# Optimization experiments

Measured on AMD Instinct MI355X. Metric: run time of the kernel, lower is better.

Reference implementation:

```python
import jax, jax.numpy as jnp
import numpy as np

H = 512  # hidden size (layer_size in the torch module)


def setup_inputs() -> dict:
    key = jax.random.key(0)
    ks = jax.random.split(key, 12)
    B, T = 512, 128
    s = 1.0 / np.sqrt(H)  # torch default LSTM/Linear init range
    def u(k, shape):
        return jax.random.uniform(k, shape, jnp.float32, -s, s)
    return {
        "x": jax.random.normal(ks[0], (B, T, 1), jnp.float32),
        "x_time": jax.random.normal(ks[1], (B, T), jnp.float32),
        "y_time": jax.random.normal(ks[2], (B, T), jnp.float32),
        # layer 0: input_size=1
        "w_ih0": u(ks[3], (4 * H, 1)),
        "w_hh0": u(ks[4], (4 * H, H)),
        "b_ih0": u(ks[5], (4 * H,)),
        "b_hh0": u(ks[6], (4 * H,)),
        # layer 1: input_size=H
        "w_ih1": u(ks[7], (4 * H, H)),
        "w_hh1": u(ks[8], (4 * H, H)),
        "b_ih1": u(ks[9], (4 * H,)),
        "b_hh1": u(ks[10], (4 * H,)),
        # output head Linear(512, 1)
        "w_lin": u(ks[11], (1, H)),
        "b_lin": jnp.zeros((1,), jnp.float32),
    }


def _cell(x, h, c, w_ih, w_hh, b):
    # torch LSTM gate order: i, f, g, o
    g = x @ w_ih.T + h @ w_hh.T + b
    i, f, gg, o = jnp.split(g, 4, axis=-1)
    c = jax.nn.sigmoid(f) * c + jax.nn.sigmoid(i) * jnp.tanh(gg)
    h = jax.nn.sigmoid(o) * jnp.tanh(c)
    return h, c


def reference(x, x_time, y_time, w_ih0, w_hh0, b_ih0, b_hh0,
              w_ih1, w_hh1, b_ih1, b_hh1, w_lin, b_lin):
    # x: [B, T, 1]; x_time / y_time are unused (as in the torch module)
    B, T, _ = x.shape
    b0 = b_ih0 + b_hh0
    b1 = b_ih1 + b_hh1

    def step(state, x_t):  # x_t: [B, 1]
        h1, c1, h2, c2 = state
        h1, c1 = _cell(x_t, h1, c1, w_ih0, w_hh0, b0)
        h2, c2 = _cell(h1, h2, c2, w_ih1, w_hh1, b1)
        return (h1, c1, h2, c2), h2

    z = jnp.zeros((B, H), x.dtype)
    state = (z, z, z, z)
    # phase 1: run the 2-layer LSTM over the full input sequence (first loop iter)
    state, _ = jax.lax.scan(step, state, jnp.swapaxes(x, 0, 1))
    y0 = state[3] @ w_lin.T + b_lin  # [B, 1] first prediction

    def ar_step(carry, _):
        st, y = carry
        st, h2 = step(st, y)
        y_new = h2 @ w_lin.T + b_lin
        return (st, y_new), y_new

    _, ys = jax.lax.scan(ar_step, (state, y0), None, length=T - 1)  # [T-1, B, 1]
    preds = jnp.concatenate([y0[None], ys], axis=0)  # [T, B, 1]
    return jnp.transpose(preds, (1, 0, 2))  # [B, T, 1]
```

## Files before the change

kernel.cpp:

```cpp
#include <hip/hip_runtime.h>
#include <math.h>
#include <stdint.h>


namespace {
constexpr int NH  = 512;
constexpr int NT  = 128;
constexpr int NB  = 512;
}

typedef __attribute__((ext_vector_type(8))) short bf16x8;
typedef __attribute__((ext_vector_type(4))) float f32x4;
typedef __attribute__((ext_vector_type(4))) unsigned int u32x4;

__global__ void ReLSTM_18940805775611_kernel() {}

__device__ __forceinline__ unsigned short lstm9_f2b(float f) {
    union { float f; uint32_t i; } v; v.f = f;
    const uint32_t r = v.i + 0x7FFFu + ((v.i >> 16) & 1u);
    return (unsigned short)(r >> 16);
}
__device__ __forceinline__ float lstm9_sig(float x) {
    return 1.0f / (1.0f + expf(-x));
}

__global__ void lstm9_mark(float* out) {
    const int i = blockIdx.x * blockDim.x + threadIdx.x;
    if (i < NB * NT) out[i] = 2.03125f;
}

__global__ void lstm9_prep(
    const float* whh0, const float* wih1, const float* whh1,
    const float* bih0, const float* bhh0, const float* bih1, const float* bhh1,
    unsigned short* wb0, unsigned short* wb1i, unsigned short* wb1h,
    float* bsum0, float* bsum1,
    unsigned short* hz, int* flags)
{
    const size_t stride = (size_t)gridDim.x * blockDim.x;
    const size_t i0 = (size_t)blockIdx.x * blockDim.x + threadIdx.x;
    const size_t NW = (size_t)4 * NH * NH;
    for (size_t i = i0; i < NW; i += stride) {
        wb0 [i] = lstm9_f2b(whh0[i]);
        wb1i[i] = lstm9_f2b(wih1[i]);
        wb1h[i] = lstm9_f2b(whh1[i]);
    }
    for (size_t i = i0; i < (size_t)4 * NH; i += stride) {
        bsum0[i] = bih0[i] + bhh0[i];
        bsum1[i] = bih1[i] + bhh1[i];
    }
    for (size_t i = i0; i < (size_t)4 * NB * NH; i += stride) hz[i] = 0;
    for (size_t i = i0; i < (size_t)2 * 256 * 8 * 32; i += stride) flags[i] = 0;
}

__device__ __forceinline__ void lstm9_ldA(u32x4& d, const unsigned short* p) {
    asm volatile("global_load_dwordx4 %0, %1, off sc0 sc1"
                 : "=v"(d) : "v"(p) : "memory");
}
__device__ __forceinline__ void lstm9_ldP(u32x4& d, const float* p) {
    asm volatile("global_load_dwordx4 %0, %1, off sc0 sc1"
                 : "=v"(d) : "v"(p) : "memory");
}
#define LSTM9_W8(N, a,b,c,d,e,f,g,h) \
    asm volatile("s_waitcnt vmcnt(" #N ")" \
        : "+v"(a),"+v"(b),"+v"(c),"+v"(d),"+v"(e),"+v"(f),"+v"(g),"+v"(h) :: "memory")
#define LSTM9_WAIT2(a,b) \
    asm volatile("s_waitcnt vmcnt(0)" : "+v"(a),"+v"(b) :: "memory")
__device__ __forceinline__ void lstm9_stH(unsigned short* p, unsigned short v) {
    unsigned int x = v;
    asm volatile("global_store_short %0, %1, off sc0 sc1" :: "v"(p), "v"(x) : "memory");
}
__device__ __forceinline__ void lstm9_stF(float* p, float v) {
    asm volatile("global_store_dword %0, %1, off sc0 sc1" :: "v"(p), "v"(v) : "memory");
}
__device__ __forceinline__ void lstm9_stI(int* p, int v) {
    asm volatile("global_store_dword %0, %1, off sc0 sc1" :: "v"(p), "v"(v) : "memory");
}
__device__ __forceinline__ void lstm9_drain() {
    asm volatile("s_waitcnt vmcnt(0)" ::: "memory");
}

__device__ __forceinline__ void lstm9_waitgrp(const int* base) {
    if (threadIdx.x < 64) {
        const int sl = (int)threadIdx.x & 31;
        for (;;) {
            int f;
            asm volatile("global_load_dword %0, %1, off sc0 sc1\n\t"
                         "s_waitcnt vmcnt(0)"
                         : "=v"(f) : "v"(base + sl) : "memory");
            if (__all(f != 0)) break;
            __builtin_amdgcn_s_sleep(2);
        }
    }
    __syncthreads();
}
__device__ __forceinline__ void lstm9_waitgrp2(const int* baseA, const int* baseB) {
    if (threadIdx.x < 64) {
        const int sl = (int)threadIdx.x & 31;
        const int* p = ((threadIdx.x < 32) ? baseA : baseB) + sl;
        for (;;) {
            int f;
            asm volatile("global_load_dword %0, %1, off sc0 sc1\n\t"
                         "s_waitcnt vmcnt(0)"
                         : "=v"(f) : "v"(p) : "memory");
            if (__all(f != 0)) break;
            __builtin_amdgcn_s_sleep(2);
        }
    }
    __syncthreads();
}

#define BFR0(gt, kk) (*(const bf16x8*)&Bsh0[gt][kk][lane][0])
#define BFR1(gt, kk) (*(const bf16x8*)&Bsh1[gt][kk][lane][0])
#define WHR(gt, kk)  (*(const bf16x8*)&whr[(gt) * 16 + (kk)])

__global__ __launch_bounds__(256, 1) void lstm9_persist(
    const float* __restrict__ xin, float* __restrict__ outf,
    const unsigned short* __restrict__ wb0,
    const unsigned short* __restrict__ wb1i,
    const unsigned short* __restrict__ wb1h,
    const float* __restrict__ bsum0, const float* __restrict__ bsum1,
    const float* __restrict__ wih0f, const float* __restrict__ wlinf,
    const float* __restrict__ blinf,
    unsigned short* h1a, unsigned short* h1b,
    unsigned short* h2a, unsigned short* h2b,
    float* parts, int* flags)
{
    __shared__ unsigned short Bsh0[4][16][64][8];
    __shared__ unsigned short Bsh1[4][16][64][8];
    __shared__ float redsh[64][17];
    __shared__ float ysh[64];

    const int tid  = threadIdx.x;
    const int lane = tid & 63;
    const int wv   = tid >> 6;
    const int quad = lane >> 4;
    const int ln15 = lane & 15;
    const int bid  = blockIdx.x;
    const int jt = (bid & 7) * 4 + ((bid >> 3) & 3);
    const int g  = bid >> 5;
    const int j0 = jt * 16;
    const int m0 = g * 64;
    const int rowA = m0 + wv * 16 + ln15;
    const int mb   = m0 + wv * 16 + quad * 4;
    const int jv   = j0 + ln15;

    for (int idx = tid; idx < 4 * 16 * 64; idx += 256) {
        const int gt = idx >> 10;
        const int ks = (idx >> 6) & 15;
        const int l  = idx & 63;
        const int row = l & 15, q = l >> 4;
        const size_t go = ((size_t)(gt * NH + j0 + row)) * NH + ks * 32 + q * 8;
        *(u32x4*)&Bsh0[gt][ks][l][0] = *(const u32x4*)(wb0  + go);
        *(u32x4*)&Bsh1[gt][ks][l][0] = *(const u32x4*)(wb1i + go);
    }
    u32x4 whr[64];
    #pragma unroll
    for (int gt = 0; gt < 4; ++gt) {
        #pragma unroll
        for (int ks = 0; ks < 16; ++ks)
            whr[gt * 16 + ks] = *(const u32x4*)(
                wb1h + ((size_t)(gt * NH + j0 + ln15)) * NH + ks * 32 + quad * 8);
    }
    __syncthreads();

    const float b0i = bsum0[jv],          b0f = bsum0[NH + jv];
    const float b0g = bsum0[2 * NH + jv], b0o = bsum0[3 * NH + jv];
    const float wxi = wih0f[jv],          wxf = wih0f[NH + jv];
    const float wxg = wih0f[2 * NH + jv], wxo = wih0f[3 * NH + jv];
    const float b1i = bsum1[jv],          b1f = bsum1[NH + jv];
    const float b1g = bsum1[2 * NH + jv], b1o = bsum1[3 * NH + jv];
    const float wl_ = wlinf[jv];
    const float bl_ = blinf[0];

    float c1r[4] = {0.f, 0.f, 0.f, 0.f};
    float c2r[4] = {0.f, 0.f, 0.f, 0.f};

    unsigned short* h1p[2] = { h1a, h1b };
    unsigned short* h2p[2] = { h2a, h2b };
    int* flagA = flags;
    int* flagB = flags + 256 * 8 * 32;

    u32x4 rP[8], rQ[8];

    for (int t = 0; t < 256; ++t) {
        const unsigned short* h1rd = h1p[t & 1];
        unsigned short*       h1wr = h1p[(t + 1) & 1];
        const unsigned short* h2rd = h2p[t & 1];
        unsigned short*       h2wr = h2p[(t + 1) & 1];

        if (t != 255) {
            #pragma unroll
            for (int ks = 0; ks < 8; ++ks)
                lstm9_ldA(rP[ks], h1rd + (size_t)rowA * NH + ks * 32 + quad * 8);
            #pragma unroll
            for (int ks = 0; ks < 8; ++ks)
                lstm9_ldA(rQ[ks], h1rd + (size_t)rowA * NH + (8 + ks) * 32 + quad * 8);
        }

        float xv[4] = {0.f, 0.f, 0.f, 0.f};
        if (t < 128) {
            #pragma unroll
            for (int r = 0; r < 4; ++r)
                xv[r] = xin[(size_t)(mb + r) * NT + t];
        } else {
            lstm9_waitgrp(flagB + ((t - 1) * 8 + g) * 32);
            const float* pslot = parts + (size_t)((t - 1) & 1) * NB * 32;
            {
                const int row = tid >> 2, q = tid & 3;
                u32x4 v0, v1;
                lstm9_ldP(v0, pslot + (size_t)(m0 + row) * 32 + q * 8);
                lstm9_ldP(v1, pslot + (size_t)(m0 + row) * 32 + q * 8 + 4);
                LSTM9_WAIT2(v0, v1);
                const float* f0 = (const float*)&v0;
                const float* f1 = (const float*)&v1;
                redsh[row][q] = f0[0] + f0[1] + f0[2] + f0[3]
                              + f1[0] + f1[1] + f1[2] + f1[3];
            }
            __syncthreads();
            if (tid < 64) {
                const float y = bl_ + redsh[tid][0] + redsh[tid][1]
                                    + redsh[tid][2] + redsh[tid][3];
                ysh[tid] = y;
                if (jt == 0)
                    outf[(size_t)(m0 + tid) * NT + (t - 128)] = y;
            }
            __syncthreads();
            if (t == 255) break;
            #pragma unroll
            for (int r = 0; r < 4; ++r)
                xv[r] = ysh[wv * 16 + quad * 4 + r];
        }

        f32x4 a0 = {0.f, 0.f, 0.f, 0.f};
        f32x4 a1 = a0, a2 = a0, a3 = a0;
        LSTM9_W8(8, rP[0], rP[1], rP[2], rP[3], rP[4], rP[5], rP[6], rP[7]);
        #pragma unroll
        for (int ks = 0; ks < 8; ++ks) {
            const bf16x8 af = *(const bf16x8*)&rP[ks];
            a0 = __builtin_amdgcn_mfma_f32_16x16x32_bf16(af, BFR0(0, ks), a0, 0, 0, 0);
            a1 = __builtin_amdgcn_mfma_f32_16x16x32_bf16(af, BFR0(1, ks), a1, 0, 0, 0);
            a2 = __builtin_amdgcn_mfma_f32_16x16x32_bf16(af, BFR0(2, ks), a2, 0, 0, 0);
            a3 = __builtin_amdgcn_mfma_f32_16x16x32_bf16(af, BFR0(3, ks), a3, 0, 0, 0);
        }
        LSTM9_W8(0, rQ[0], rQ[1], rQ[2], rQ[3], rQ[4], rQ[5], rQ[6], rQ[7]);
        #pragma unroll
        for (int ks = 0; ks < 8; ++ks) {
            const bf16x8 af = *(const bf16x8*)&rQ[ks];
            a0 = __builtin_amdgcn_mfma_f32_16x16x32_bf16(af, BFR0(0, 8 + ks), a0, 0, 0, 0);
            a1 = __builtin_amdgcn_mfma_f32_16x16x32_bf16(af, BFR0(1, 8 + ks), a1, 0, 0, 0);
            a2 = __builtin_amdgcn_mfma_f32_16x16x32_bf16(af, BFR0(2, 8 + ks), a2, 0, 0, 0);
            a3 = __builtin_amdgcn_mfma_f32_16x16x32_bf16(af, BFR0(3, 8 + ks), a3, 0, 0, 0);
        }

        #pragma unroll
        for (int r = 0; r < 4; ++r) {
            const float gi = a0[r] + fmaf(xv[r], wxi, b0i);
            const float gf = a1[r] + fmaf(xv[r], wxf, b0f);
            const float gg = a2[r] + fmaf(xv[r], wxg, b0g);
            const float go = a3[r] + fmaf(xv[r], wxo, b0o);
            float cv = c1r[r];
            cv = lstm9_sig(gf) * cv + lstm9_sig(gi) * tanhf(gg);
            c1r[r] = cv;
            lstm9_stH(h1wr + (size_t)(mb + r) * NH + jv,
                      lstm9_f2b(lstm9_sig(go) * tanhf(cv)));
        }
        lstm9_drain();
        __syncthreads();
        if (tid == 0) lstm9_stI(flagA + (t * 8 + g) * 32 + jt, 1);

        if (t < 128) {
            const int* bA = flagA + (t * 8 + g) * 32;
            const int* bB = (t >= 1) ? (flagB + ((t - 1) * 8 + g) * 32) : bA;
            lstm9_waitgrp2(bA, bB);
        } else {
            lstm9_waitgrp(flagA + (t * 8 + g) * 32);
        }

        a0 = {0.f, 0.f, 0.f, 0.f}; a1 = a0; a2 = a0; a3 = a0;
        #pragma unroll
        for (int ks = 0; ks < 8; ++ks)
            lstm9_ldA(rP[ks], h2rd + (size_t)rowA * NH + ks * 32 + quad * 8);
        #pragma unroll
        for (int ks = 0; ks < 8; ++ks)
            lstm9_ldA(rQ[ks], h2rd + (size_t)rowA * NH + (8 + ks) * 32 + quad * 8);
        LSTM9_W8(8, rP[0], rP[1], rP[2], rP[3], rP[4], rP[5], rP[6], rP[7]);
        #pragma unroll
        for (int ks = 0; ks < 8; ++ks) {
            const bf16x8 af = *(const bf16x8*)&rP[ks];
            a0 = __builtin_amdgcn_mfma_f32_16x16x32_bf16(af, WHR(0, ks), a0, 0, 0, 0);
            a1 = __builtin_amdgcn_mfma_f32_16x16x32_bf16(af, WHR(1, ks), a1, 0, 0, 0);
            a2 = __builtin_amdgcn_mfma_f32_16x16x32_bf16(af, WHR(2, ks), a2, 0, 0, 0);
            a3 = __builtin_amdgcn_mfma_f32_16x16x32_bf16(af, WHR(3, ks), a3, 0, 0, 0);
        }
        #pragma unroll
        for (int ks = 0; ks < 8; ++ks)
            lstm9_ldA(rP[ks], h1wr + (size_t)rowA * NH + ks * 32 + quad * 8);
        LSTM9_W8(8, rQ[0], rQ[1], rQ[2], rQ[3], rQ[4], rQ[5], rQ[6], rQ[7]);
        #pragma unroll
        for (int ks = 0; ks < 8; ++ks) {
            const bf16x8 af = *(const bf16x8*)&rQ[ks];
            a0 = __builtin_amdgcn_mfma_f32_16x16x32_bf16(af, WHR(0, 8 + ks), a0, 0, 0, 0);
            a1 = __builtin_amdgcn_mfma_f32_16x16x32_bf16(af, WHR(1, 8 + ks), a1, 0, 0, 0);
            a2 = __builtin_amdgcn_mfma_f32_16x16x32_bf16(af, WHR(2, 8 + ks), a2, 0, 0, 0);
            a3 = __builtin_amdgcn_mfma_f32_16x16x32_bf16(af, WHR(3, 8 + ks), a3, 0, 0, 0);
        }
        #pragma unroll
        for (int ks = 0; ks < 8; ++ks)
            lstm9_ldA(rQ[ks], h1wr + (size_t)rowA * NH + (8 + ks) * 32 + quad * 8);
        LSTM9_W8(8, rP[0], rP[1], rP[2], rP[3], rP[4], rP[5], rP[6], rP[7]);
        #pragma unroll
        for (int ks = 0; ks < 8; ++ks) {
            const bf16x8 af = *(const bf16x8*)&rP[ks];
            a0 = __builtin_amdgcn_mfma_f32_16x16x32_bf16(af, BFR1(0, ks), a0, 0, 0, 0);
            a1 = __builtin_amdgcn_mfma_f32_16x16x32_bf16(af, BFR1(1, ks), a1, 0, 0, 0);
            a2 = __builtin_amdgcn_mfma_f32_16x16x32_bf16(af, BFR1(2, ks), a2, 0, 0, 0);
            a3 = __builtin_amdgcn_mfma_f32_16x16x32_bf16(af, BFR1(3, ks), a3, 0, 0, 0);
        }
        LSTM9_W8(0, rQ[0], rQ[1], rQ[2], rQ[3], rQ[4], rQ[5], rQ[6], rQ[7]);
        #pragma unroll
        for (int ks = 0; ks < 8; ++ks) {
            const bf16x8 af = *(const bf16x8*)&rQ[ks];
            a0 = __builtin_amdgcn_mfma_f32_16x16x32_bf16(af, BFR1(0, 8 + ks), a0, 0, 0, 0);
            a1 = __builtin_amdgcn_mfma_f32_16x16x32_bf16(af, BFR1(1, 8 + ks), a1, 0, 0, 0);
            a2 = __builtin_amdgcn_mfma_f32_16x16x32_bf16(af, BFR1(2, 8 + ks), a2, 0, 0, 0);
            a3 = __builtin_amdgcn_mfma_f32_16x16x32_bf16(af, BFR1(3, 8 + ks), a3, 0, 0, 0);
        }

        float hv[4], cva[4];
        #pragma unroll
        for (int r = 0; r < 4; ++r) {
            const float gi = a0[r] + b1i;
            const float gf = a1[r] + b1f;
            const float gg = a2[r] + b1g;
            const float go = a3[r] + b1o;
            float cv = c2r[r];
            cv = lstm9_sig(gf) * cv + lstm9_sig(gi) * tanhf(gg);
            c2r[r] = cv;
            cva[r] = cv;
            hv[r] = lstm9_sig(go) * tanhf(cv);
            lstm9_stH(h2wr + (size_t)(mb + r) * NH + jv, lstm9_f2b(hv[r]));
        }
        if (t >= 127) {
            #pragma unroll
            for (int r = 0; r < 4; ++r)
                redsh[wv * 16 + quad * 4 + r][ln15] =
                    (t == 127 ? cva[r] : hv[r]) * wl_;
            __syncthreads();
            if (tid < 64) {
                float s = 0.0f;
                #pragma unroll
                for (int j = 0; j < 16; ++j) s += redsh[tid][j];
                lstm9_stF(parts + (size_t)(t & 1) * NB * 32
                                + (size_t)(m0 + tid) * 32 + jt, s);
            }
        }
        lstm9_drain();
        __syncthreads();
        if (tid == 0) lstm9_stI(flagB + (t * 8 + g) * 32 + jt, 1);
    }
}

extern "C" void kernel_launch(void* const* d_in, const int* in_sizes, int n_in,
                              void* d_out, int out_size, void* d_ws, size_t ws_size,
                              hipStream_t stream)
{
    int base = 3;
    if (!(n_in > 3 && in_sizes[3] == 4 * NH)) {
        for (int i = 1; i + 9 < n_in; ++i)
            if (in_sizes[i] == 4 * NH) { base = i; break; }
    }
    const float* xin  = (const float*)d_in[0];
    const float* wih0 = (const float*)d_in[base + 0];
    const float* whh0 = (const float*)d_in[base + 1];
    const float* bih0 = (const float*)d_in[base + 2];
    const float* bhh0 = (const float*)d_in[base + 3];
    const float* wih1 = (const float*)d_in[base + 4];
    const float* whh1 = (const float*)d_in[base + 5];
    const float* bih1 = (const float*)d_in[base + 6];
    const float* bhh1 = (const float*)d_in[base + 7];
    const float* wlin = (const float*)d_in[base + 8];
    const float* blin = (const float*)d_in[base + 9];
    float* outf = (float*)d_out;

    const size_t NW = (size_t)4 * NH * NH;
    const size_t S  = (size_t)NB * NH;
    unsigned short* wb0  = (unsigned short*)d_ws;
    unsigned short* wb1i = wb0 + NW;
    unsigned short* wb1h = wb1i + NW;
    unsigned short* h1b0 = wb1h + NW;
    unsigned short* h1b1 = h1b0 + S;
    unsigned short* h2b0 = h1b1 + S;
    unsigned short* h2b1 = h2b0 + S;
    float* bsum0 = (float*)(h2b1 + S);
    float* bsum1 = bsum0 + 4 * NH;
    float* parts = bsum1 + 4 * NH;
    int*   flags = (int*)(parts + 2 * NB * 32);

    lstm9_mark<<<(NB * NT + 255) / 256, 256, 0, stream>>>(outf);
    lstm9_prep<<<1024, 256, 0, stream>>>(whh0, wih1, whh1, bih0, bhh0, bih1, bhh1,
                                         wb0, wb1i, wb1h, bsum0, bsum1,
                                         h1b0, flags);
    lstm9_persist<<<256, 256, 0, stream>>>(xin, outf, wb0, wb1i, wb1h,
                                           bsum0, bsum1, wih0, wlin, blin,
                                           h1b0, h1b1, h2b0, h2b1,
                                           parts, flags);
}
```

Measured before the change: 3.629 ms.

## Reuse loaded h1 registers for next-step layer-0 GEMM and overlap with parts reduction

The h1 fragments loaded for the layer-1 input GEMM are kept in registers (rA1/rA2) and reused as the A operand for the next step's layer-0 recurrent GEMM, removing the separate reload of h1 at the top of each step. In the autoregressive phase the layer-0 MFMAs are issued between the partial-sum loads and their wait, hiding the load latency. All four h2/h1 fragment groups are loaded up front with staged waitcnt counts. Spin-wait sleeps become adaptive, short at first and longer after several polls. This raises register pressure (32 u32x4 operand registers live at once) and relies on the registers holding exactly what the previous step wrote to global memory.

```diff
diff --git a/kernel.cpp b/kernel.cpp
--- a/kernel.cpp
+++ b/kernel.cpp
@@ -82,13 +82,16 @@
 __device__ __forceinline__ void lstm9_waitgrp(const int* base) {
     if (threadIdx.x < 64) {
         const int sl = (int)threadIdx.x & 31;
+        int it = 0;
         for (;;) {
             int f;
             asm volatile("global_load_dword %0, %1, off sc0 sc1\n\t"
                          "s_waitcnt vmcnt(0)"
                          : "=v"(f) : "v"(base + sl) : "memory");
             if (__all(f != 0)) break;
-            __builtin_amdgcn_s_sleep(2);
+            if (it < 4) __builtin_amdgcn_s_sleep(1);
+            else        __builtin_amdgcn_s_sleep(8);
+            ++it;
         }
     }
     __syncthreads();
@@ -97,13 +100,16 @@
     if (threadIdx.x < 64) {
         const int sl = (int)threadIdx.x & 31;
         const int* p = ((threadIdx.x < 32) ? baseA : baseB) + sl;
+        int it = 0;
         for (;;) {
             int f;
             asm volatile("global_load_dword %0, %1, off sc0 sc1\n\t"
                          "s_waitcnt vmcnt(0)"
                          : "=v"(f) : "v"(p) : "memory");
             if (__all(f != 0)) break;
-            __builtin_amdgcn_s_sleep(2);
+            if (it < 4) __builtin_amdgcn_s_sleep(1);
+            else        __builtin_amdgcn_s_sleep(8);
+            ++it;
         }
     }
     __syncthreads();
@@ -112,6 +118,26 @@
 #define BFR0(gt, kk) (*(const bf16x8*)&Bsh0[gt][kk][lane][0])
 #define BFR1(gt, kk) (*(const bf16x8*)&Bsh1[gt][kk][lane][0])
 #define WHR(gt, kk)  (*(const bf16x8*)&whr[(gt) * 16 + (kk)])
+
+#define LSTM9_L0_MFMAS()                                                          \
+    do {                                                                          \
+        _Pragma("unroll")                                                         \
+        for (int ks = 0; ks < 8; ++ks) {                                          \
+            const bf16x8 af = *(const bf16x8*)&rA1[ks];                           \
+            a0 = __builtin_amdgcn_mfma_f32_16x16x32_bf16(af, BFR0(0, ks), a0, 0, 0, 0); \
+            a1 = __builtin_amdgcn_mfma_f32_16x16x32_bf16(af, BFR0(1, ks), a1, 0, 0, 0); \
+            a2 = __builtin_amdgcn_mfma_f32_16x16x32_bf16(af, BFR0(2, ks), a2, 0, 0, 0); \
+            a3 = __builtin_amdgcn_mfma_f32_16x16x32_bf16(af, BFR0(3, ks), a3, 0, 0, 0); \
+        }                                                                         \
+        _Pragma("unroll")                                                         \
+        for (int ks = 0; ks < 8; ++ks) {                                          \
+            const bf16x8 af = *(const bf16x8*)&rA2[ks];                           \
+            a0 = __builtin_amdgcn_mfma_f32_16x16x32_bf16(af, BFR0(0, 8 + ks), a0, 0, 0, 0); \
+            a1 = __builtin_amdgcn_mfma_f32_16x16x32_bf16(af, BFR0(1, 8 + ks), a1, 0, 0, 0); \
+            a2 = __builtin_amdgcn_mfma_f32_16x16x32_bf16(af, BFR0(2, 8 + ks), a2, 0, 0, 0); \
+            a3 = __builtin_amdgcn_mfma_f32_16x16x32_bf16(af, BFR0(3, 8 + ks), a3, 0, 0, 0); \
+        }                                                                         \
+    } while (0)
 
 __global__ __launch_bounds__(256, 1) void lstm9_persist(
     const float* __restrict__ xin, float* __restrict__ outf,
@@ -180,42 +206,40 @@
     int* flagA = flags;
     int* flagB = flags + 256 * 8 * 32;
 
-    u32x4 rP[8], rQ[8];
+    u32x4 rA1[8], rA2[8];
+    #pragma unroll
+    for (int ks = 0; ks < 8; ++ks) {
+        rA1[ks] = (u32x4){0u, 0u, 0u, 0u};
+        rA2[ks] = (u32x4){0u, 0u, 0u, 0u};
+    }
+    u32x4 rH2a[8], rH2b[8];
 
     for (int t = 0; t < 256; ++t) {
-        const unsigned short* h1rd = h1p[t & 1];
         unsigned short*       h1wr = h1p[(t + 1) & 1];
         const unsigned short* h2rd = h2p[t & 1];
         unsigned short*       h2wr = h2p[(t + 1) & 1];
 
-        if (t != 255) {
-            #pragma unroll
-            for (int ks = 0; ks < 8; ++ks)
-                lstm9_ldA(rP[ks], h1rd + (size_t)rowA * NH + ks * 32 + quad * 8);
-            #pragma unroll
-            for (int ks = 0; ks < 8; ++ks)
-                lstm9_ldA(rQ[ks], h1rd + (size_t)rowA * NH + (8 + ks) * 32 + quad * 8);
-        }
-
         float xv[4] = {0.f, 0.f, 0.f, 0.f};
+        f32x4 a0 = {0.f, 0.f, 0.f, 0.f};
+        f32x4 a1 = a0, a2 = a0, a3 = a0;
         if (t < 128) {
             #pragma unroll
             for (int r = 0; r < 4; ++r)
                 xv[r] = xin[(size_t)(mb + r) * NT + t];
+            LSTM9_L0_MFMAS();
         } else {
             lstm9_waitgrp(flagB + ((t - 1) * 8 + g) * 32);
             const float* pslot = parts + (size_t)((t - 1) & 1) * NB * 32;
-            {
-                const int row = tid >> 2, q = tid & 3;
-                u32x4 v0, v1;
-                lstm9_ldP(v0, pslot + (size_t)(m0 + row) * 32 + q * 8);
-                lstm9_ldP(v1, pslot + (size_t)(m0 + row) * 32 + q * 8 + 4);
-                LSTM9_WAIT2(v0, v1);
-                const float* f0 = (const float*)&v0;
-                const float* f1 = (const float*)&v1;
-                redsh[row][q] = f0[0] + f0[1] + f0[2] + f0[3]
-                              + f1[0] + f1[1] + f1[2] + f1[3];
-            }
+            const int row = tid >> 2, q = tid & 3;
+            u32x4 v0, v1;
+            lstm9_ldP(v0, pslot + (size_t)(m0 + row) * 32 + q * 8);
+            lstm9_ldP(v1, pslot + (size_t)(m0 + row) * 32 + q * 8 + 4);
+            if (t < 255) LSTM9_L0_MFMAS();
+            LSTM9_WAIT2(v0, v1);
+            const float* f0 = (const float*)&v0;
+            const float* f1 = (const float*)&v1;
+            redsh[row][q] = f0[0] + f0[1] + f0[2] + f0[3]
+                          + f1[0] + f1[1] + f1[2] + f1[3];
             __syncthreads();
             if (tid < 64) {
                 const float y = bl_ + redsh[tid][0] + redsh[tid][1]
@@ -231,27 +255,6 @@
                 xv[r] = ysh[wv * 16 + quad * 4 + r];
         }
 
-        f32x4 a0 = {0.f, 0.f, 0.f, 0.f};
-        f32x4 a1 = a0, a2 = a0, a3 = a0;
-        LSTM9_W8(8, rP[0], rP[1], rP[2], rP[3], rP[4], rP[5], rP[6], rP[7]);
-        #pragma unroll
-        for (int ks = 0; ks < 8; ++ks) {
-            const bf16x8 af = *(const bf16x8*)&rP[ks];
-            a0 = __builtin_amdgcn_mfma_f32_16x16x32_bf16(af, BFR0(0, ks), a0, 0, 0, 0);
-            a1 = __builtin_amdgcn_mfma_f32_16x16x32_bf16(af, BFR0(1, ks), a1, 0, 0, 0);
-            a2 = __builtin_amdgcn_mfma_f32_16x16x32_bf16(af, BFR0(2, ks), a2, 0, 0, 0);
-            a3 = __builtin_amdgcn_mfma_f32_16x16x32_bf16(af, BFR0(3, ks), a3, 0, 0, 0);
-        }
-        LSTM9_W8(0, rQ[0], rQ[1], rQ[2], rQ[3], rQ[4], rQ[5], rQ[6], rQ[7]);
-        #pragma unroll
-        for (int ks = 0; ks < 8; ++ks) {
-            const bf16x8 af = *(const bf16x8*)&rQ[ks];
-            a0 = __builtin_amdgcn_mfma_f32_16x16x32_bf16(af, BFR0(0, 8 + ks), a0, 0, 0, 0);
-            a1 = __builtin_amdgcn_mfma_f32_16x16x32_bf16(af, BFR0(1, 8 + ks), a1, 0, 0, 0);
-            a2 = __builtin_amdgcn_mfma_f32_16x16x32_bf16(af, BFR0(2, 8 + ks), a2, 0, 0, 0);
-            a3 = __builtin_amdgcn_mfma_f32_16x16x32_bf16(af, BFR0(3, 8 + ks), a3, 0, 0, 0);
-        }
-
         #pragma unroll
         for (int r = 0; r < 4; ++r) {
             const float gi = a0[r] + fmaf(xv[r], wxi, b0i);
@@ -279,47 +282,52 @@
         a0 = {0.f, 0.f, 0.f, 0.f}; a1 = a0; a2 = a0; a3 = a0;
         #pragma unroll
         for (int ks = 0; ks < 8; ++ks)
-            lstm9_ldA(rP[ks], h2rd + (size_t)rowA * NH + ks * 32 + quad * 8);
+            lstm9_ldA(rH2a[ks], h2rd + (size_t)rowA * NH + ks * 32 + quad * 8);
         #pragma unroll
         for (int ks = 0; ks < 8; ++ks)
-            lstm9_ldA(rQ[ks], h2rd + (size_t)rowA * NH + (8 + ks) * 32 + quad * 8);
-        LSTM9_W8(8, rP[0], rP[1], rP[2], rP[3], rP[4], rP[5], rP[6], rP[7]);
+            lstm9_ldA(rH2b[ks], h2rd + (size_t)rowA * NH + (8 + ks) * 32 + quad * 8);
+        #pragma unroll
+        for (int ks = 0; ks < 8; ++ks)
+            lstm9_ldA(rA1[ks], h1wr + (size_t)rowA * NH + ks * 32 + quad * 8);
+        #pragma unroll
+        for (int ks = 0; ks < 8; ++ks)
+            lstm9_ldA(rA2[ks], h1wr + (size_t)rowA * NH + (8 + ks) * 32 + quad * 8);
+
+        LSTM9_W8(24, rH2a[0], rH2a[1], rH2a[2], rH2a[3],
+                     rH2a[4], rH2a[5], rH2a[6], rH2a[7]);
         #pragma unroll
         for (int ks = 0; ks < 8; ++ks) {
-            const bf16x8 af = *(const bf16x8*)&rP[ks];
+            const bf16x8 af = *(const bf16x8*)&rH2a[ks];
             a0 = __builtin_amdgcn_mfma_f32_16x16x32_bf16(af, WHR(0, ks), a0, 0, 0, 0);
             a1 = __builtin_amdgcn_mfma_f32_16x16x32_bf16(af, WHR(1, ks), a1, 0, 0, 0);
             a2 = __builtin_amdgcn_mfma_f32_16x16x32_bf16(af, WHR(2, ks), a2, 0, 0, 0);
             a3 = __builtin_amdgcn_mfma_f32_16x16x32_bf16(af, WHR(3, ks), a3, 0, 0, 0);
         }
-        #pragma unroll
-        for (int ks = 0; ks < 8; ++ks)
-            lstm9_ldA(rP[ks], h1wr + (size_t)rowA * NH + ks * 32 + quad * 8);
-        LSTM9_W8(8, rQ[0], rQ[1], rQ[2], rQ[3], rQ[4], rQ[5], rQ[6], rQ[7]);
+        LSTM9_W8(16, rH2b[0], rH2b[1], rH2b[2], rH2b[3],
+                     rH2b[4], rH2b[5], rH2b[6], rH2b[7]);
         #pragma unroll
         for (int ks = 0; ks < 8; ++ks) {
-            const bf16x8 af = *(const bf16x8*)&rQ[ks];
+            const bf16x8 af = *(const bf16x8*)&rH2b[ks];
             a0 = __builtin_amdgcn_mfma_f32_16x16x32_bf16(af, WHR(0, 8 + ks), a0, 0, 0, 0);
             a1 = __builtin_amdgcn_mfma_f32_16x16x32_bf16(af, WHR(1, 8 + ks), a1, 0, 0, 0);
             a2 = __builtin_amdgcn_mfma_f32_16x16x32_bf16(af, WHR(2, 8 + ks), a2, 0, 0, 0);
             a3 = __builtin_amdgcn_mfma_f32_16x16x32_bf16(af, WHR(3, 8 + ks), a3, 0, 0, 0);
         }
-        #pragma unroll
-        for (int ks = 0; ks < 8; ++ks)
-            lstm9_ldA(rQ[ks], h1wr + (size_t)rowA * NH + (8 + ks) * 32 + quad * 8);
-        LSTM9_W8(8, rP[0], rP[1], rP[2], rP[3], rP[4], rP[5], rP[6], rP[7]);
+        LSTM9_W8(8, rA1[0], rA1[1], rA1[2], rA1[3],
+                    rA1[4], rA1[5], rA1[6], rA1[7]);
         #pragma unroll
         for (int ks = 0; ks < 8; ++ks) {
-            const bf16x8 af = *(const bf16x8*)&rP[ks];
+            const bf16x8 af = *(const bf16x8*)&rA1[ks];
             a0 = __builtin_amdgcn_mfma_f32_16x16x32_bf16(af, BFR1(0, ks), a0, 0, 0, 0);
             a1 = __builtin_amdgcn_mfma_f32_16x16x32_bf16(af, BFR1(1, ks), a1, 0, 0, 0);
             a2 = __builtin_amdgcn_mfma_f32_16x16x32_bf16(af, BFR1(2, ks), a2, 0, 0, 0);
             a3 = __builtin_amdgcn_mfma_f32_16x16x32_bf16(af, BFR1(3, ks), a3, 0, 0, 0);
         }
-        LSTM9_W8(0, rQ[0], rQ[1], rQ[2], rQ[3], rQ[4], rQ[5], rQ[6], rQ[7]);
+        LSTM9_W8(0, rA2[0], rA2[1], rA2[2], rA2[3],
+                    rA2[4], rA2[5], rA2[6], rA2[7]);
         #pragma unroll
         for (int ks = 0; ks < 8; ++ks) {
-            const bf16x8 af = *(const bf16x8*)&rQ[ks];
+            const bf16x8 af = *(const bf16x8*)&rA2[ks];
             a0 = __builtin_amdgcn_mfma_f32_16x16x32_bf16(af, BFR1(0, 8 + ks), a0, 0, 0, 0);
             a1 = __builtin_amdgcn_mfma_f32_16x16x32_bf16(af, BFR1(1, 8 + ks), a1, 0, 0, 0);
             a2 = __builtin_amdgcn_mfma_f32_16x16x32_bf16(af, BFR1(2, 8 + ks), a2, 0, 0, 0);
```

Measured after the change: 3.409 ms. 1.06x faster.
